# Optimization experiments

Measured on AMD Instinct MI355X. Metric: run time of the kernel, lower is better.

Reference implementation:

```python
import jax, jax.numpy as jnp
import numpy as np

N = 20000; E = 320000; IN = 128; H = 6; C = 64; HC = H * C; NC = 16; NG = 64


def _gatv2(x, src, dst, wl, bl, wr, br, att, bias, heads, out_c, concat):
    # PyG GATv2Conv (eval mode, share_weights=False, negative_slope=0.2)
    n = x.shape[0]
    xl = (x @ wl + bl).reshape(n, heads, out_c)   # source-side transform
    xr = (x @ wr + br).reshape(n, heads, out_c)   # target-side transform
    # edge-wise attention logits: leaky_relu(x_l[j] + x_r[i]) . att
    e = jnp.einsum('ehc,hc->eh', jax.nn.leaky_relu(xl[src] + xr[dst], 0.2), att)
    # segment softmax over incoming edges of each target node
    emax = jax.ops.segment_max(e, dst, num_segments=n)
    a = jnp.exp(e - emax[dst])
    denom = jax.ops.segment_sum(a, dst, num_segments=n)
    alpha = a / (denom[dst] + 1e-16)
    out = jax.ops.segment_sum(xl[src] * alpha[:, :, None], dst, num_segments=n)
    out = out.reshape(n, heads * out_c) if concat else out.mean(axis=1)
    return out + bias


def setup_inputs() -> dict:
    key = jax.random.key(0)
    ks = jax.random.split(key, 32)
    s = 0.05
    inp = {}
    inp['x'] = jax.random.normal(ks[0], (N, IN), jnp.float32)
    inp['edge_index'] = jax.random.randint(ks[1], (2, E), 0, N, dtype=jnp.int32)
    inp['batch'] = jnp.sort(jax.random.randint(ks[2], (N,), 0, NG, dtype=jnp.int32))
    # input projection (input_dim != hidden_dim * n_heads)
    inp['inp_w'] = jax.random.normal(ks[3], (IN, HC), jnp.float32) * s
    inp['inp_b'] = jnp.zeros((HC,), jnp.float32)
    # layer 0: IN -> (H, C), concat
    inp['l0_wl'] = jax.random.normal(ks[4], (IN, HC), jnp.float32) * s
    inp['l0_bl'] = jnp.zeros((HC,), jnp.float32)
    inp['l0_wr'] = jax.random.normal(ks[5], (IN, HC), jnp.float32) * s
    inp['l0_br'] = jnp.zeros((HC,), jnp.float32)
    inp['l0_att'] = jax.random.normal(ks[6], (H, C), jnp.float32) * s
    inp['l0_bias'] = jnp.zeros((HC,), jnp.float32)
    # layer 1: HC -> (H, C), concat
    inp['l1_wl'] = jax.random.normal(ks[7], (HC, HC), jnp.float32) * s
    inp['l1_bl'] = jnp.zeros((HC,), jnp.float32)
    inp['l1_wr'] = jax.random.normal(ks[8], (HC, HC), jnp.float32) * s
    inp['l1_br'] = jnp.zeros((HC,), jnp.float32)
    inp['l1_att'] = jax.random.normal(ks[9], (H, C), jnp.float32) * s
    inp['l1_bias'] = jnp.zeros((HC,), jnp.float32)
    # layer 2: HC -> (1, C), no concat (mean over the single head)
    inp['l2_wl'] = jax.random.normal(ks[10], (HC, C), jnp.float32) * s
    inp['l2_bl'] = jnp.zeros((C,), jnp.float32)
    inp['l2_wr'] = jax.random.normal(ks[11], (HC, C), jnp.float32) * s
    inp['l2_br'] = jnp.zeros((C,), jnp.float32)
    inp['l2_att'] = jax.random.normal(ks[12], (1, C), jnp.float32) * s
    inp['l2_bias'] = jnp.zeros((C,), jnp.float32)
    # residual projection HC -> C at the last layer (bias-free Linear)
    inp['res_w'] = jax.random.normal(ks[13], (HC, C), jnp.float32) * s
    # dense head: Linear(C,C) + BatchNorm1d(eval) + ReLU + Linear(C,NC)
    inp['d1_w'] = jax.random.normal(ks[14], (C, C), jnp.float32) * s
    inp['d1_b'] = jnp.zeros((C,), jnp.float32)
    inp['bn_g'] = jnp.ones((C,), jnp.float32)
    inp['bn_b'] = jnp.zeros((C,), jnp.float32)
    inp['bn_m'] = jnp.zeros((C,), jnp.float32)
    inp['bn_v'] = jnp.ones((C,), jnp.float32)
    inp['d2_w'] = jax.random.normal(ks[15], (C, NC), jnp.float32) * s
    inp['d2_b'] = jnp.zeros((NC,), jnp.float32)
    return inp


def reference(x, edge_index, batch, inp_w, inp_b,
              l0_wl, l0_bl, l0_wr, l0_br, l0_att, l0_bias,
              l1_wl, l1_bl, l1_wr, l1_br, l1_att, l1_bias,
              l2_wl, l2_bl, l2_wr, l2_br, l2_att, l2_bias,
              res_w, d1_w, d1_b, bn_g, bn_b, bn_m, bn_v, d2_w, d2_b):
    n = x.shape[0]
    sl = jnp.arange(n, dtype=edge_index.dtype)           # self-loops (PyG default)
    src = jnp.concatenate([edge_index[0], sl])
    dst = jnp.concatenate([edge_index[1], sl])
    x_res = x @ inp_w + inp_b
    h = jax.nn.elu(_gatv2(x, src, dst, l0_wl, l0_bl, l0_wr, l0_br, l0_att, l0_bias, H, C, True)) + x_res
    x_res = h
    h = jax.nn.elu(_gatv2(h, src, dst, l1_wl, l1_bl, l1_wr, l1_br, l1_att, l1_bias, H, C, True)) + x_res
    x_res = h
    h = jax.nn.elu(_gatv2(h, src, dst, l2_wl, l2_bl, l2_wr, l2_br, l2_att, l2_bias, 1, C, False)) + x_res @ res_w
    pooled = jax.ops.segment_sum(h, batch, num_segments=NG)
    z = pooled @ d1_w + d1_b
    z = (z - bn_m) / jnp.sqrt(bn_v + 1e-5) * bn_g + bn_b  # BatchNorm1d eval
    z = jax.nn.relu(z) @ d2_w + d2_b
    return h, z
```

## Files before the change

kernel.cpp:

```cpp
#include <hip/hip_runtime.h>
#include <hip/hip_bf16.h>
#include <math.h>

#define NN 20000
#define EE 320000
#define IND 128
#define HH 6
#define CC 64
#define HCC 384
#define NCC 16
#define NGG 64

typedef __bf16 bf16x8 __attribute__((ext_vector_type(8)));
typedef float f32x4 __attribute__((ext_vector_type(4)));
typedef float f32x2 __attribute__((ext_vector_type(2)));
typedef unsigned short ushort_t;
typedef unsigned int uint_t;

#define LOG2E 1.44269504088896f

__device__ inline ushort_t f2bf(float f) {
    union { float f; uint_t u; } x; x.f = f;
    uint_t r = (x.u + 0x7FFF + ((x.u >> 16) & 1)) >> 16;
    return (ushort_t)r;
}
__device__ inline void bf8cvt2(uint4 v, f32x2* f) {
    union { uint_t u; float x; } a, b;
    a.u = v.x << 16; b.u = v.x & 0xFFFF0000u; f[0] = (f32x2){a.x, b.x};
    a.u = v.y << 16; b.u = v.y & 0xFFFF0000u; f[1] = (f32x2){a.x, b.x};
    a.u = v.z << 16; b.u = v.z & 0xFFFF0000u; f[2] = (f32x2){a.x, b.x};
    a.u = v.w << 16; b.u = v.w & 0xFFFF0000u; f[3] = (f32x2){a.x, b.x};
}

template <int CTRL>
__device__ inline float dppadd(float x) {
    int y = __builtin_amdgcn_mov_dpp(__builtin_bit_cast(int, x), CTRL, 0xF, 0xF, true);
    return x + __builtin_bit_cast(float, y);
}

__device__ inline void load_lds16(const ushort_t* g, ushort_t* l) {
    __builtin_amdgcn_global_load_lds(
        (const __attribute__((address_space(1))) void*)g,
        (__attribute__((address_space(3))) void*)l, 16, 0, 0);
}

__device__ inline int xcd_swz(int lin, int nwg) {
    int q = nwg >> 3, r = nwg & 7;
    int xc = lin & 7, j = lin >> 3;
    return (xc < r ? xc * (q + 1) : r * (q + 1) + (xc - r) * q) + j;
}


__global__ void zero_init_kernel(int* counts, int* s6_tail, int* s1_tail,
                                 float* pooled, int n, int np) {
    int t = blockIdx.x * blockDim.x + threadIdx.x;
    if (t < n) counts[t] = 0;
    if (t < np) pooled[t] = 0.0f;
    if (t < 8) { s6_tail[t] = 0; s1_tail[t] = 0; }
}

__global__ void count_kernel(const int* __restrict__ ei, int* __restrict__ counts, int E) {
    int t = blockIdx.x * blockDim.x + threadIdx.x;
    if (t < E) atomicAdd(&counts[ei[E + t]], 1);
}

__global__ __launch_bounds__(1024) void scan_kernel(
    const int* __restrict__ counts, int* __restrict__ offsets,
    int* __restrict__ cursor, int n) {
    __shared__ int buf[NN];
    __shared__ int part[1024];
    int t = threadIdx.x;
    for (int idx = t; idx < n; idx += 1024) buf[idx] = counts[idx] + 1;
    __syncthreads();
    int per = (n + 1023) / 1024;
    int base = t * per;
    int sum = 0;
    for (int j = 0; j < per; ++j) {
        int idx = base + j;
        if (idx < n) sum += buf[idx];
    }
    part[t] = sum;
    __syncthreads();
    for (int off = 1; off < 1024; off <<= 1) {
        int v = (t >= off) ? part[t - off] : 0;
        __syncthreads();
        part[t] += v;
        __syncthreads();
    }
    int run = (t == 0) ? 0 : part[t - 1];
    for (int j = 0; j < per; ++j) {
        int idx = base + j;
        if (idx < n) {
            int deg = buf[idx];
            buf[idx] = run;
            run += deg;
        }
    }
    __syncthreads();
    for (int idx = t; idx < n; idx += 1024) {
        int v = buf[idx];
        offsets[idx] = v;
        cursor[idx] = v;
    }
    if (t == 1023) offsets[n] = run;
}

__global__ void fill_kernel(const int* __restrict__ ei, int* __restrict__ cursor,
                            int* __restrict__ srcs6, int* __restrict__ srcs1,
                            int E, int n) {
    int t = blockIdx.x * blockDim.x + threadIdx.x;
    if (t < E) {
        int s = ei[t];
        int d = ei[E + t];
        int slot = atomicAdd(&cursor[d], 1);
        srcs6[slot] = s * 1536;
        srcs1[slot] = s << 8;
    } else if (t < E + n) {
        int i = t - E;
        int slot = atomicAdd(&cursor[i], 1);
        srcs6[slot] = i * 1536;
        srcs1[slot] = i << 8;
    }
}

#define WBIG (1152 * IND)
#define WC1 (768 * HCC)
#define WC2 (192 * HCC)
#define XB_N (NN * IND)
#define PREP_TOTAL (WBIG + WC1 + WC2 + XB_N + 1152 + 768 + 192)

__global__ void prep_kernel(const float* __restrict__ x, const float* __restrict__ inp_w,
    const float* __restrict__ l0wl, const float* __restrict__ l0wr,
    const float* __restrict__ l1wl, const float* __restrict__ l1wr,
    const float* __restrict__ l2wl, const float* __restrict__ l2wr,
    const float* __restrict__ resw,
    const float* __restrict__ inp_b,
    const float* __restrict__ l0bl, const float* __restrict__ l0br,
    const float* __restrict__ l1bl, const float* __restrict__ l1br,
    const float* __restrict__ l2bl, const float* __restrict__ l2br,
    ushort_t* wBig, ushort_t* wC1, ushort_t* wC2, ushort_t* xb,
    float* bBig, float* bC1, float* bC2)
{
    int i = blockIdx.x * blockDim.x + threadIdx.x;
    if (i >= PREP_TOTAL) return;
    if (i < WBIG) {
        int col = i >> 7, k = i & 127;
        float v;
        if (col < 384)      v = inp_w[k * 384 + col];
        else if (col < 768) v = l0wl[k * 384 + (col - 384)];
        else                v = l0wr[k * 384 + (col - 768)];
        wBig[i] = f2bf(v); return;
    }
    i -= WBIG;
    if (i < WC1) {
        int col = i / 384, k = i - col * 384;
        float v = col < 384 ? l1wl[k * 384 + col] : l1wr[k * 384 + (col - 384)];
        wC1[i] = f2bf(v); return;
    }
    i -= WC1;
    if (i < WC2) {
        int col = i / 384, k = i - col * 384;
        float v;
        if (col < 64)       v = resw[k * 64 + col];
        else if (col < 128) v = l2wl[k * 64 + (col - 64)];
        else                v = l2wr[k * 64 + (col - 128)];
        wC2[i] = f2bf(v); return;
    }
    i -= WC2;
    if (i < XB_N) { xb[i] = f2bf(x[i]); return; }
    i -= XB_N;
    if (i < 1152) {
        float v;
        if (i < 384)      v = inp_b[i];
        else if (i < 768) v = l0bl[i - 384];
        else              v = l0br[i - 768];
        bBig[i] = v; return;
    }
    i -= 1152;
    if (i < 768) { bC1[i] = i < 384 ? l1bl[i] : l1br[i - 384]; return; }
    i -= 768;
    if (i < 192) {
        float v;
        if (i < 64)       v = 0.0f;
        else if (i < 128) v = l2bl[i - 64];
        else              v = l2br[i - 128];
        bC2[i] = v; return;
    }
}

__global__ __launch_bounds__(512) void gemm_mfma2(
    const ushort_t* __restrict__ A, const ushort_t* __restrict__ BT,
    const float* __restrict__ bias,
    ushort_t* __restrict__ Cb1, int ld1,
    ushort_t* __restrict__ Cb2, int ld2, int split,
    int M, int N, int K, int NT)
{
    __shared__ ushort_t Bs[2][2][128 * 32];
    int t = threadIdx.x;
    int w = t >> 6, L = t & 63;
    int nwg = gridDim.x * gridDim.y;
    int logical = xcd_swz(blockIdx.y * gridDim.x + blockIdx.x, nwg);
    int bx = logical % gridDim.x;
    int by = logical / gridDim.x;
    int m0 = bx * 256;
    int q = L >> 4, r16 = L & 15;
    int lr = L >> 2;
    int lc = ((L & 3) ^ ((lr >> 1) & 3)) * 8;
    int sw = (q ^ ((r16 >> 1) & 3)) * 8;
    int oB = (w * 16) * 32;

    int rA0 = min(m0 + w * 32 + r16, M - 1);
    int rA1 = min(m0 + w * 32 + 16 + r16, M - 1);
    const ushort_t* pA0base = A + (size_t)rA0 * K + q * 8;
    const ushort_t* pA1base = A + (size_t)rA1 * K + q * 8;

    for (int nt = 0; nt < NT; ++nt) {
        int n0 = (by * NT + nt) * 128;
        int rB = min(n0 + w * 16 + lr, N - 1);
        const ushort_t* gB = BT + (size_t)rB * K + lc;
        const ushort_t* pA0 = pA0base;
        const ushort_t* pA1 = pA1base;

        f32x4 acc[2][8];
#pragma unroll
        for (int a = 0; a < 2; ++a)
#pragma unroll
            for (int b = 0; b < 8; ++b) acc[a][b] = (f32x4){0.f, 0.f, 0.f, 0.f};

        load_lds16(gB, &Bs[0][0][oB]);
        load_lds16(gB + 32, &Bs[0][1][oB]);
        gB += 64;
        bf16x8 a0 = *(const bf16x8*)pA0;
        bf16x8 a2 = *(const bf16x8*)(pA0 + 32);
        bf16x8 a1 = *(const bf16x8*)pA1;
        bf16x8 a3 = *(const bf16x8*)(pA1 + 32);
        pA0 += 64; pA1 += 64;

        int buf = 0;
        for (int k0 = 0; k0 < K; k0 += 64) {
            __syncthreads();
            bool more = (k0 + 64 < K);
            if (more) {
                int nb = buf ^ 1;
                load_lds16(gB, &Bs[nb][0][oB]);
                load_lds16(gB + 32, &Bs[nb][1][oB]);
                gB += 64;
            }
            bf16x8 na0, na1, na2, na3;
            if (more) {
                na0 = *(const bf16x8*)pA0;
                na2 = *(const bf16x8*)(pA0 + 32);
                na1 = *(const bf16x8*)pA1;
                na3 = *(const bf16x8*)(pA1 + 32);
                pA0 += 64; pA1 += 64;
            }
#pragma unroll
            for (int ct = 0; ct < 8; ++ct) {
                bf16x8 blo = *(const bf16x8*)&Bs[buf][0][(ct * 16 + r16) * 32 + sw];
                bf16x8 bhi = *(const bf16x8*)&Bs[buf][1][(ct * 16 + r16) * 32 + sw];
                acc[0][ct] = __builtin_amdgcn_mfma_f32_16x16x32_bf16(blo, a0, acc[0][ct], 0, 0, 0);
                acc[1][ct] = __builtin_amdgcn_mfma_f32_16x16x32_bf16(blo, a1, acc[1][ct], 0, 0, 0);
                acc[0][ct] = __builtin_amdgcn_mfma_f32_16x16x32_bf16(bhi, a2, acc[0][ct], 0, 0, 0);
                acc[1][ct] = __builtin_amdgcn_mfma_f32_16x16x32_bf16(bhi, a3, acc[1][ct], 0, 0, 0);
            }
            if (more) { a0 = na0; a1 = na1; a2 = na2; a3 = na3; }
            buf ^= 1;
        }
#pragma unroll
        for (int rt = 0; rt < 2; ++rt) {
            int row = m0 + w * 32 + rt * 16 + r16;
            if (row >= M) continue;
#pragma unroll
            for (int ct = 0; ct < 8; ++ct) {
                int colb = n0 + ct * 16 + q * 4;
                if (colb >= N) continue;
                float4 bv = *(const float4*)(bias + colb);
                uint2 pk;
                pk.x = (uint_t)f2bf(acc[rt][ct][0] + bv.x) | ((uint_t)f2bf(acc[rt][ct][1] + bv.y) << 16);
                pk.y = (uint_t)f2bf(acc[rt][ct][2] + bv.z) | ((uint_t)f2bf(acc[rt][ct][3] + bv.w) << 16);
                if (colb < split)
                    *(uint2*)(Cb1 + (size_t)row * ld1 + colb) = pk;
                else
                    *(uint2*)(Cb2 + (size_t)row * ld2 + (colb - split)) = pk;
            }
        }
    }
}

__global__ __launch_bounds__(256) void gemm_mfma(
    const ushort_t* __restrict__ A, const ushort_t* __restrict__ BT,
    const float* __restrict__ bias,
    float* __restrict__ Cf, ushort_t* __restrict__ Cb1, int ld1,
    ushort_t* __restrict__ Cb2, int ld2, int split,
    int M, int N, int K)
{
    __shared__ ushort_t Bs[2][2][128 * 32];
    int t = threadIdx.x;
    int w = t >> 6, L = t & 63;
    int nwg = gridDim.x * gridDim.y;
    int logical = xcd_swz(blockIdx.y * gridDim.x + blockIdx.x, nwg);
    int m0 = (logical % gridDim.x) * 128;
    int n0 = (logical / gridDim.x) * 128;
    int q = L >> 4, r16 = L & 15;

    f32x4 acc[2][8];
#pragma unroll
    for (int a = 0; a < 2; ++a)
#pragma unroll
        for (int b = 0; b < 8; ++b) acc[a][b] = (f32x4){0.f, 0.f, 0.f, 0.f};

    int lr = L >> 2;
    int lc = ((L & 3) ^ ((lr >> 1) & 3)) * 8;
    int rB0 = min(n0 + w * 32 + lr, N - 1);
    int rB1 = min(n0 + w * 32 + 16 + lr, N - 1);
    const ushort_t* gB0 = BT + (size_t)rB0 * K + lc;
    const ushort_t* gB1 = BT + (size_t)rB1 * K + lc;
    int oB0 = (w * 32) * 32;
    int oB1 = (w * 32 + 16) * 32;

    int rA0 = min(m0 + w * 32 + r16, M - 1);
    int rA1 = min(m0 + w * 32 + 16 + r16, M - 1);
    const ushort_t* pA0 = A + (size_t)rA0 * K + q * 8;
    const ushort_t* pA1 = A + (size_t)rA1 * K + q * 8;

    int sw = (q ^ ((r16 >> 1) & 3)) * 8;

    load_lds16(gB0, &Bs[0][0][oB0]);
    load_lds16(gB1, &Bs[0][0][oB1]);
    load_lds16(gB0 + 32, &Bs[0][1][oB0]);
    load_lds16(gB1 + 32, &Bs[0][1][oB1]);
    gB0 += 64; gB1 += 64;
    bf16x8 a0 = *(const bf16x8*)pA0;
    bf16x8 a2 = *(const bf16x8*)(pA0 + 32);
    bf16x8 a1 = *(const bf16x8*)pA1;
    bf16x8 a3 = *(const bf16x8*)(pA1 + 32);
    pA0 += 64; pA1 += 64;

    int buf = 0;
    for (int k0 = 0; k0 < K; k0 += 64) {
        __syncthreads();
        bool more = (k0 + 64 < K);
        if (more) {
            int nb = buf ^ 1;
            load_lds16(gB0, &Bs[nb][0][oB0]);
            load_lds16(gB1, &Bs[nb][0][oB1]);
            load_lds16(gB0 + 32, &Bs[nb][1][oB0]);
            load_lds16(gB1 + 32, &Bs[nb][1][oB1]);
            gB0 += 64; gB1 += 64;
        }
        bf16x8 na0, na1, na2, na3;
        if (more) {
            na0 = *(const bf16x8*)pA0;
            na2 = *(const bf16x8*)(pA0 + 32);
            na1 = *(const bf16x8*)pA1;
            na3 = *(const bf16x8*)(pA1 + 32);
            pA0 += 64; pA1 += 64;
        }
#pragma unroll
        for (int ct = 0; ct < 8; ++ct) {
            bf16x8 blo = *(const bf16x8*)&Bs[buf][0][(ct * 16 + r16) * 32 + sw];
            bf16x8 bhi = *(const bf16x8*)&Bs[buf][1][(ct * 16 + r16) * 32 + sw];
            acc[0][ct] = __builtin_amdgcn_mfma_f32_16x16x32_bf16(blo, a0, acc[0][ct], 0, 0, 0);
            acc[1][ct] = __builtin_amdgcn_mfma_f32_16x16x32_bf16(blo, a1, acc[1][ct], 0, 0, 0);
            acc[0][ct] = __builtin_amdgcn_mfma_f32_16x16x32_bf16(bhi, a2, acc[0][ct], 0, 0, 0);
            acc[1][ct] = __builtin_amdgcn_mfma_f32_16x16x32_bf16(bhi, a3, acc[1][ct], 0, 0, 0);
        }
        if (more) { a0 = na0; a1 = na1; a2 = na2; a3 = na3; }
        buf ^= 1;
    }
#pragma unroll
    for (int rt = 0; rt < 2; ++rt) {
        int row = m0 + w * 32 + rt * 16 + r16;
        if (row >= M) continue;
#pragma unroll
        for (int ct = 0; ct < 8; ++ct) {
            int colb = n0 + ct * 16 + q * 4;
            if (colb >= N) continue;
            float4 bv = *(const float4*)(bias + colb);
            float v0 = acc[rt][ct][0] + bv.x;
            float v1 = acc[rt][ct][1] + bv.y;
            float v2 = acc[rt][ct][2] + bv.z;
            float v3 = acc[rt][ct][3] + bv.w;
            if (colb < split) {
                if (Cf) {
                    *(float4*)(Cf + (size_t)row * ld1 + colb) = make_float4(v0, v1, v2, v3);
                } else {
                    uint2 pk;
                    pk.x = (uint_t)f2bf(v0) | ((uint_t)f2bf(v1) << 16);
                    pk.y = (uint_t)f2bf(v2) | ((uint_t)f2bf(v3) << 16);
                    *(uint2*)(Cb1 + (size_t)row * ld1 + colb) = pk;
                }
            } else {
                uint2 pk;
                pk.x = (uint_t)f2bf(v0) | ((uint_t)f2bf(v1) << 16);
                pk.y = (uint_t)f2bf(v2) | ((uint_t)f2bf(v3) << 16);
                *(uint2*)(Cb2 + (size_t)row * ld2 + (colb - split)) = pk;
            }
        }
    }
}

__global__ __launch_bounds__(128) void gat6_kernel(
    const ushort_t* __restrict__ cat, const float* __restrict__ att,
    const float* __restrict__ bias, const ushort_t* __restrict__ resB,
    ushort_t* __restrict__ outB,
    const int* __restrict__ offsets, const int* __restrict__ srcs6, int n)
{
    int wid = (blockIdx.x * blockDim.x + threadIdx.x) >> 6;
    if (wid >= n) return;
    int lane = threadIdx.x & 63;
    int h = lane >> 3, c8 = lane & 7;
    bool hv = h < HH;
    int off = h * 64 + c8 * 8;
    int offL2 = (hv ? off : off - 384) * 2;
    int i = wid;
    int beg = __builtin_amdgcn_readfirstlane(offsets[i]);
    int end = __builtin_amdgcn_readfirstlane(offsets[i + 1]);
    int deg = end - beg;
    int P = (deg + 1) >> 1;
    const char* catc = (const char*)cat;

    f32x2 xr2[4], att2[4];
    {
        uint4 v = *(const uint4*)(catc + (size_t)i * 1536 + 768 + offL2);
        bf8cvt2(v, xr2);
    }
#pragma unroll
    for (int j = 0; j < 4; ++j) {
        int o = (offL2 >> 1) + 2 * j;
        att2[j] = (f32x2){att[o] * LOG2E, att[o + 1] * LOG2E};
    }

    float s = 0.0f;
    f32x2 acc2[4];
#pragma unroll
    for (int j = 0; j < 4; ++j) acc2[j] = (f32x2){0.f, 0.f};

    int bA0 = srcs6[beg], bB0 = srcs6[beg + 1];
    uint4 cA = *(const uint4*)(catc + (size_t)(uint_t)bA0 + offL2);
    uint4 cB = *(const uint4*)(catc + (size_t)(uint_t)bB0 + offL2);
    int iA1 = srcs6[beg + 2], iB1 = srcs6[beg + 3];

    for (int p = 0; p < P; ++p) {
        uint4 nA = cA, nB = cB;
        bool pre = (p + 1 < P);
        if (pre) {
            nA = *(const uint4*)(catc + (size_t)(uint_t)iA1 + offL2);
            nB = *(const uint4*)(catc + (size_t)(uint_t)iB1 + offL2);
            iA1 = srcs6[beg + 2 * p + 4];
            iB1 = srcs6[beg + 2 * p + 5];
        }
        f32x2 xlA[4], xlB[4];
        bf8cvt2(cA, xlA);
        bf8cvt2(cB, xlB);
        f32x2 pA2 = (f32x2){0.f, 0.f}, pB2 = (f32x2){0.f, 0.f};
#pragma unroll
        for (int j = 0; j < 4; ++j) {
            f32x2 ta = xlA[j] + xr2[j];
            ta = __builtin_elementwise_max(ta, ta * 0.2f);
            pA2 += ta * att2[j];
            f32x2 tb = xlB[j] + xr2[j];
            tb = __builtin_elementwise_max(tb, tb * 0.2f);
            pB2 += tb * att2[j];
        }
        float pA = pA2.x + pA2.y, pB = pB2.x + pB2.y;
        pA = dppadd<0xB1>(pA);
        pB = dppadd<0xB1>(pB);
        pA = dppadd<0x4E>(pA);
        pB = dppadd<0x4E>(pB);
        pA = dppadd<0x141>(pA);
        pB = dppadd<0x141>(pB);
        float wA = __builtin_amdgcn_exp2f(pA);
        float wB = (2 * p + 1 < deg) ? __builtin_amdgcn_exp2f(pB) : 0.0f;
        s += wA + wB;
        f32x2 wA2 = (f32x2){wA, wA}, wB2 = (f32x2){wB, wB};
#pragma unroll
        for (int j = 0; j < 4; ++j) {
            acc2[j] += wA2 * xlA[j];
            acc2[j] += wB2 * xlB[j];
        }
        cA = nA; cB = nB;
    }

    if (hv) {
        float inv = 1.0f / (s + 1e-16f);
        size_t ob = (size_t)i * HCC + off;
        uint4 rv = *(const uint4*)(resB + ob);
        f32x2 rr[4];
        bf8cvt2(rv, rr);
        ushort_t u[8];
#pragma unroll
        for (int j = 0; j < 4; ++j) {
            float v0 = acc2[j].x * inv + bias[off + 2 * j];
            float v1 = acc2[j].y * inv + bias[off + 2 * j + 1];
            v0 = v0 > 0.0f ? v0 : expm1f(v0);
            v1 = v1 > 0.0f ? v1 : expm1f(v1);
            u[2 * j]     = f2bf(v0 + rr[j].x);
            u[2 * j + 1] = f2bf(v1 + rr[j].y);
        }
        *(uint4*)(outB + ob) = *(uint4*)u;
    }
}

__global__ __launch_bounds__(128) void gat1_kernel(
    const ushort_t* __restrict__ cat, const float* __restrict__ att,
    const float* __restrict__ bias, const float* __restrict__ res,
    float* __restrict__ out,
    const int* __restrict__ offsets, const int* __restrict__ srcs1, int n)
{
    int wid = (blockIdx.x * blockDim.x + threadIdx.x) >> 6;
    if (wid >= n) return;
    int lane = threadIdx.x & 63;
    int e8 = lane >> 3, c8 = lane & 7;
    int i = wid;
    int beg = __builtin_amdgcn_readfirstlane(offsets[i]);
    int end = __builtin_amdgcn_readfirstlane(offsets[i + 1]);
    const char* catc = (const char*)cat;

    f32x2 xr2[4], att2[4];
    {
        uint4 v = *(const uint4*)(cat + (size_t)i * 128 + 64 + c8 * 8);
        bf8cvt2(v, xr2);
    }
#pragma unroll
    for (int j = 0; j < 4; ++j)
        att2[j] = (f32x2){att[c8 * 8 + 2 * j] * LOG2E, att[c8 * 8 + 2 * j + 1] * LOG2E};

    float s = 0.0f;
    f32x2 acc2[4];
#pragma unroll
    for (int j = 0; j < 4; ++j) acc2[j] = (f32x2){0.f, 0.f};

    const uint4 z = make_uint4(0u, 0u, 0u, 0u);
    int p = beg + e8;
    bool val = p < end;
    int b = val ? srcs1[p] : (i << 8);
    uint4 v = *(const uint4*)(catc + (size_t)(uint_t)b + c8 * 16);

    for (int p0 = beg; p0 < end; p0 += 8) {
        uint4 nv = z;
        bool nval = false;
        if (p0 + 8 < end) {
            int np = p0 + 8 + e8;
            nval = np < end;
            int nb = nval ? srcs1[np] : (i << 8);
            nv = *(const uint4*)(catc + (size_t)(uint_t)nb + c8 * 16);
        }
        f32x2 xl[4];
        bf8cvt2(v, xl);
        f32x2 pp2 = (f32x2){0.f, 0.f};
#pragma unroll
        for (int j = 0; j < 4; ++j) {
            f32x2 tv = xl[j] + xr2[j];
            tv = __builtin_elementwise_max(tv, tv * 0.2f);
            pp2 += tv * att2[j];
        }
        float partial = pp2.x + pp2.y;
        partial = dppadd<0xB1>(partial);
        partial = dppadd<0x4E>(partial);
        partial = dppadd<0x141>(partial);
        float wE = val ? __builtin_amdgcn_exp2f(partial) : 0.0f;
        s += wE;
        f32x2 w2 = (f32x2){wE, wE};
#pragma unroll
        for (int j = 0; j < 4; ++j) acc2[j] += w2 * xl[j];
        v = nv;
        val = nval;
    }

    s = dppadd<0x140>(s);
    s += __shfl_xor(s, 16, 64);
    s += __shfl_xor(s, 32, 64);
#pragma unroll
    for (int j = 0; j < 4; ++j) {
        acc2[j].x += __shfl_xor(acc2[j].x, 8, 64);
        acc2[j].y += __shfl_xor(acc2[j].y, 8, 64);
        acc2[j].x += __shfl_xor(acc2[j].x, 16, 64);
        acc2[j].y += __shfl_xor(acc2[j].y, 16, 64);
        acc2[j].x += __shfl_xor(acc2[j].x, 32, 64);
        acc2[j].y += __shfl_xor(acc2[j].y, 32, 64);
    }
    if (e8 == 0) {
        float inv = 1.0f / (s + 1e-16f);
        size_t ob = (size_t)i * CC + c8 * 8;
        float4 r0 = *(const float4*)(res + ob);
        float4 r1 = *(const float4*)(res + ob + 4);
        float rr[8] = {r0.x, r0.y, r0.z, r0.w, r1.x, r1.y, r1.z, r1.w};
        float av[8] = {acc2[0].x, acc2[0].y, acc2[1].x, acc2[1].y,
                       acc2[2].x, acc2[2].y, acc2[3].x, acc2[3].y};
#pragma unroll
        for (int j = 0; j < 8; ++j) {
            float v2 = av[j] * inv + bias[c8 * 8 + j];
            v2 = v2 > 0.0f ? v2 : expm1f(v2);
            av[j] = v2 + rr[j];
        }
        *(float4*)(out + ob) = make_float4(av[0], av[1], av[2], av[3]);
        *(float4*)(out + ob + 4) = make_float4(av[4], av[5], av[6], av[7]);
    }
}

__global__ __launch_bounds__(256) void pool_kernel(const float* __restrict__ h,
                                                   const int* __restrict__ batch,
                                                   float* __restrict__ pooled, int n) {
    int b = blockIdx.x;
    int g = b >> 2, qd = b & 3;
    int t = threadIdx.x;
    int w = t >> 6, lane = t & 63;
    int lo = 0, hi = n;
    while (lo < hi) { int mid = (lo + hi) >> 1; if (batch[mid] < g) lo = mid + 1; else hi = mid; }
    int start = lo;
    int hi2 = n;
    while (lo < hi2) { int mid = (lo + hi2) >> 1; if (batch[mid] < g + 1) lo = mid + 1; else hi2 = mid; }
    int endd = lo;
    int len = endd - start;
    int q0 = start + (len * qd) / 4;
    int q1 = start + (len * (qd + 1)) / 4;
    float acc = 0.0f;
    for (int r = q0 + w; r < q1; r += 4)
        acc += h[(size_t)r * 64 + lane];
    __shared__ float red[4][64];
    red[w][lane] = acc;
    __syncthreads();
    if (w == 0) {
        float v2 = red[0][lane] + red[1][lane] + red[2][lane] + red[3][lane];
        atomicAdd(&pooled[g * 64 + lane], v2);
    }
}

__global__ __launch_bounds__(256) void head_kernel(const float* __restrict__ pooled,
                            const float* __restrict__ d1w, const float* __restrict__ d1b,
                            const float* __restrict__ bng, const float* __restrict__ bnb,
                            const float* __restrict__ bnm, const float* __restrict__ bnv,
                            const float* __restrict__ d2w, const float* __restrict__ d2b,
                            float* __restrict__ zout) {
    __shared__ float pl[64 * 64];
    __shared__ float w1[64 * 64];
    __shared__ float w2[64 * NCC];
    __shared__ float z1[64 * 64];
    int t = threadIdx.x;
    for (int i = t * 4; i < 64 * 64; i += 1024) {
        *(float4*)&pl[i] = *(const float4*)&pooled[i];
        *(float4*)&w1[i] = *(const float4*)&d1w[i];
    }
    for (int i = t * 4; i < 64 * NCC; i += 1024)
        *(float4*)&w2[i] = *(const float4*)&d2w[i];
    __syncthreads();
    for (int idx = t; idx < 64 * 64; idx += 256) {
        int r = idx >> 6, c = idx & 63;
        float acc = d1b[c];
        for (int k = 0; k < 64; ++k) acc += pl[r * 64 + k] * w1[k * 64 + c];
        acc = (acc - bnm[c]) / sqrtf(bnv[c] + 1e-5f) * bng[c] + bnb[c];
        z1[idx] = acc > 0.0f ? acc : 0.0f;
    }
    __syncthreads();
    for (int idx = t; idx < 64 * NCC; idx += 256) {
        int r = idx >> 4, c = idx & 15;
        float acc = d2b[c];
        for (int k = 0; k < 64; ++k) acc += z1[r * 64 + k] * w2[k * NCC + c];
        zout[idx] = acc;
    }
}


extern "C" void kernel_launch(void* const* d_in, const int* in_sizes, int n_in,
                              void* d_out, int out_size, void* d_ws, size_t ws_size,
                              hipStream_t stream) {
    const int N = NN, E = EE, C = CC, HC = HCC, NG = NGG;
    const int EN = E + N;

    const float* x     = (const float*)d_in[0];
    const int*   ei    = (const int*)d_in[1];
    const int*   batch = (const int*)d_in[2];
    const float* inp_w = (const float*)d_in[3];
    const float* inp_b = (const float*)d_in[4];
    const float* l0_wl = (const float*)d_in[5];
    const float* l0_bl = (const float*)d_in[6];
    const float* l0_wr = (const float*)d_in[7];
    const float* l0_br = (const float*)d_in[8];
    const float* l0_att = (const float*)d_in[9];
    const float* l0_bias = (const float*)d_in[10];
    const float* l1_wl = (const float*)d_in[11];
    const float* l1_bl = (const float*)d_in[12];
    const float* l1_wr = (const float*)d_in[13];
    const float* l1_br = (const float*)d_in[14];
    const float* l1_att = (const float*)d_in[15];
    const float* l1_bias = (const float*)d_in[16];
    const float* l2_wl = (const float*)d_in[17];
    const float* l2_bl = (const float*)d_in[18];
    const float* l2_wr = (const float*)d_in[19];
    const float* l2_br = (const float*)d_in[20];
    const float* l2_att = (const float*)d_in[21];
    const float* l2_bias = (const float*)d_in[22];
    const float* res_w = (const float*)d_in[23];
    const float* d1_w = (const float*)d_in[24];
    const float* d1_b = (const float*)d_in[25];
    const float* bn_g = (const float*)d_in[26];
    const float* bn_b = (const float*)d_in[27];
    const float* bn_m = (const float*)d_in[28];
    const float* bn_v = (const float*)d_in[29];
    const float* d2_w = (const float*)d_in[30];
    const float* d2_b = (const float*)d_in[31];

    float* out = (float*)d_out;

    char* ws = (char*)d_ws;
    size_t off = 0;
    auto alloc = [&](size_t bytes) -> void* {
        void* p = ws + off;
        off += (bytes + 255) & ~(size_t)255;
        return p;
    };
    ushort_t* bufH_b  = (ushort_t*)alloc((size_t)N * HC * 2);
    ushort_t* cat01_b = (ushort_t*)alloc((size_t)N * 768 * 2 + 2048);
    ushort_t* xres_b  = (ushort_t*)alloc((size_t)N * HC * 2);
    ushort_t* cat2_b  = (ushort_t*)alloc((size_t)N * 128 * 2);
    float*    bufRes  = (float*)alloc((size_t)N * C * 4);
    ushort_t* xb      = (ushort_t*)alloc((size_t)N * IND * 2);
    ushort_t* wBig    = (ushort_t*)alloc((size_t)WBIG * 2);
    ushort_t* wC1     = (ushort_t*)alloc((size_t)WC1 * 2);
    ushort_t* wC2     = (ushort_t*)alloc((size_t)WC2 * 2);
    float*    bBig    = (float*)alloc((size_t)1152 * 4);
    float*    bC1     = (float*)alloc((size_t)768 * 4);
    float*    bC2     = (float*)alloc((size_t)192 * 4);
    int*      counts  = (int*)alloc((size_t)N * 4);
    int*      cursor  = (int*)alloc((size_t)N * 4);
    int*      offsets = (int*)alloc((size_t)(N + 1) * 4);
    int*      srcs6   = (int*)alloc((size_t)(EN + 8) * 4);
    int*      srcs1   = (int*)alloc((size_t)(EN + 8) * 4);
    float*    pooled  = (float*)alloc((size_t)NG * C * 4);

    zero_init_kernel<<<(N + 255) / 256, 256, 0, stream>>>(counts, srcs6 + EN, srcs1 + EN,
                                                          pooled, N, NG * C);
    count_kernel<<<(E + 255) / 256, 256, 0, stream>>>(ei, counts, E);
    scan_kernel<<<1, 1024, 0, stream>>>(counts, offsets, cursor, N);
    fill_kernel<<<(EN + 255) / 256, 256, 0, stream>>>(ei, cursor, srcs6, srcs1, E, N);
    prep_kernel<<<(PREP_TOTAL + 255) / 256, 256, 0, stream>>>(
        x, inp_w, l0_wl, l0_wr, l1_wl, l1_wr, l2_wl, l2_wr, res_w,
        inp_b, l0_bl, l0_br, l1_bl, l1_br, l2_bl, l2_br,
        wBig, wC1, wC2, xb, bBig, bC1, bC2);

    int mtiles256 = (N + 255) / 256;
    int mtiles = (N + 127) / 128;
    dim3 gblk(128);
    int gatBlocks = (N * 64 + 127) / 128;

    gemm_mfma2<<<dim3(mtiles256, 3), dim3(512), 0, stream>>>(xb, wBig, bBig,
        xres_b, HC, cat01_b, 768, 384, N, 1152, IND, 3);
    gat6_kernel<<<gatBlocks, gblk, 0, stream>>>(cat01_b, l0_att, l0_bias,
                                                xres_b, bufH_b, offsets, srcs6, N);
    gemm_mfma2<<<dim3(mtiles256, 3), dim3(512), 0, stream>>>(bufH_b, wC1, bC1,
        nullptr, 0, cat01_b, 768, 0, N, 768, HC, 2);
    gat6_kernel<<<gatBlocks, gblk, 0, stream>>>(cat01_b, l1_att, l1_bias,
                                                bufH_b, bufH_b, offsets, srcs6, N);
    gemm_mfma<<<dim3(mtiles, 2), dim3(256), 0, stream>>>(bufH_b, wC2, bC2,
        bufRes, nullptr, C, cat2_b, 128, 64, N, 192, HC);
    gat1_kernel<<<gatBlocks, gblk, 0, stream>>>(cat2_b, l2_att, l2_bias,
                                                bufRes, out, offsets, srcs1, N);
    pool_kernel<<<NG * 4, 256, 0, stream>>>(out, batch, pooled, N);
    head_kernel<<<1, 256, 0, stream>>>(pooled, d1_w, d1_b, bn_g, bn_b, bn_m, bn_v,
                                       d2_w, d2_b, out + (size_t)N * C);
}
```

Measured before the change: 402.6 us.

## Parallelize CSR offset scan across blocks, merge source index arrays, reorder GEMM tiles

```diff
diff --git a/kernel.cpp b/kernel.cpp
--- a/kernel.cpp
+++ b/kernel.cpp
@@ -51,12 +51,12 @@
 }
 
 
-__global__ void zero_init_kernel(int* counts, int* s6_tail, int* s1_tail,
+__global__ void zero_init_kernel(int* counts, int* srcs_tail,
                                  float* pooled, int n, int np) {
     int t = blockIdx.x * blockDim.x + threadIdx.x;
     if (t < n) counts[t] = 0;
     if (t < np) pooled[t] = 0.0f;
-    if (t < 8) { s6_tail[t] = 0; s1_tail[t] = 0; }
+    if (t < 8) srcs_tail[t] = 0;
 }
 
 __global__ void count_kernel(const int* __restrict__ ei, int* __restrict__ counts, int E) {
@@ -64,62 +64,58 @@
     if (t < E) atomicAdd(&counts[ei[E + t]], 1);
 }
 
-__global__ __launch_bounds__(1024) void scan_kernel(
+__global__ __launch_bounds__(256) void scan_local_kernel(
     const int* __restrict__ counts, int* __restrict__ offsets,
-    int* __restrict__ cursor, int n) {
-    __shared__ int buf[NN];
-    __shared__ int part[1024];
-    int t = threadIdx.x;
-    for (int idx = t; idx < n; idx += 1024) buf[idx] = counts[idx] + 1;
+    int* __restrict__ blockSums, int n) {
+    __shared__ int lp[256];
+    int t = threadIdx.x, b = blockIdx.x;
+    int i = b * 256 + t;
+    int v = (i < n) ? counts[i] + 1 : 0;
+    lp[t] = v;
     __syncthreads();
-    int per = (n + 1023) / 1024;
-    int base = t * per;
-    int sum = 0;
-    for (int j = 0; j < per; ++j) {
-        int idx = base + j;
-        if (idx < n) sum += buf[idx];
-    }
-    part[t] = sum;
+    for (int o = 1; o < 256; o <<= 1) {
+        int u = (t >= o) ? lp[t - o] : 0;
+        __syncthreads();
+        lp[t] += u;
+        __syncthreads();
+    }
+    if (t == 255) blockSums[b] = lp[255];
+    if (i < n) offsets[i] = lp[t] - v;
+}
+
+__global__ __launch_bounds__(256) void scan_fixup_kernel(
+    const int* __restrict__ blockSums,
+    int* __restrict__ offsets, int* __restrict__ cursor, int n, int nb) {
+    __shared__ int red[256];
+    int t = threadIdx.x, b = blockIdx.x;
+    red[t] = (t < b) ? blockSums[t] : 0;
     __syncthreads();
-    for (int off = 1; off < 1024; off <<= 1) {
-        int v = (t >= off) ? part[t - off] : 0;
+    for (int o = 128; o > 0; o >>= 1) {
+        if (t < o) red[t] += red[t + o];
         __syncthreads();
-        part[t] += v;
-        __syncthreads();
-    }
-    int run = (t == 0) ? 0 : part[t - 1];
-    for (int j = 0; j < per; ++j) {
-        int idx = base + j;
-        if (idx < n) {
-            int deg = buf[idx];
-            buf[idx] = run;
-            run += deg;
-        }
-    }
-    __syncthreads();
-    for (int idx = t; idx < n; idx += 1024) {
-        int v = buf[idx];
-        offsets[idx] = v;
-        cursor[idx] = v;
-    }
-    if (t == 1023) offsets[n] = run;
+    }
+    int prefix = red[0];
+    int i = b * 256 + t;
+    if (i < n) {
+        int val = offsets[i] + prefix;
+        offsets[i] = val;
+        cursor[i] = val;
+    }
+    if (b == nb - 1 && t == 0) offsets[n] = prefix + blockSums[b];
 }
 
 __global__ void fill_kernel(const int* __restrict__ ei, int* __restrict__ cursor,
-                            int* __restrict__ srcs6, int* __restrict__ srcs1,
-                            int E, int n) {
+                            int* __restrict__ srcs, int E, int n) {
     int t = blockIdx.x * blockDim.x + threadIdx.x;
     if (t < E) {
         int s = ei[t];
         int d = ei[E + t];
         int slot = atomicAdd(&cursor[d], 1);
-        srcs6[slot] = s * 1536;
-        srcs1[slot] = s << 8;
+        srcs[slot] = s << 8;
     } else if (t < E + n) {
         int i = t - E;
         int slot = atomicAdd(&cursor[i], 1);
-        srcs6[slot] = i * 1536;
-        srcs1[slot] = i << 8;
+        srcs[slot] = i << 8;
     }
 }
 
@@ -200,8 +196,8 @@
     int w = t >> 6, L = t & 63;
     int nwg = gridDim.x * gridDim.y;
     int logical = xcd_swz(blockIdx.y * gridDim.x + blockIdx.x, nwg);
-    int bx = logical % gridDim.x;
-    int by = logical / gridDim.x;
+    int bx = logical / gridDim.y;
+    int by = logical % gridDim.y;
     int m0 = bx * 256;
     int q = L >> 4, r16 = L & 15;
     int lr = L >> 2;
@@ -299,8 +295,8 @@
     int w = t >> 6, L = t & 63;
     int nwg = gridDim.x * gridDim.y;
     int logical = xcd_swz(blockIdx.y * gridDim.x + blockIdx.x, nwg);
-    int m0 = (logical % gridDim.x) * 128;
-    int n0 = (logical / gridDim.x) * 128;
+    int m0 = (logical / gridDim.y) * 128;
+    int n0 = (logical % gridDim.y) * 128;
     int q = L >> 4, r16 = L & 15;
 
     f32x4 acc[2][8];
@@ -404,7 +400,7 @@
     const ushort_t* __restrict__ cat, const float* __restrict__ att,
     const float* __restrict__ bias, const ushort_t* __restrict__ resB,
     ushort_t* __restrict__ outB,
-    const int* __restrict__ offsets, const int* __restrict__ srcs6, int n)
+    const int* __restrict__ offsets, const int* __restrict__ srcs, int n)
 {
     int wid = (blockIdx.x * blockDim.x + threadIdx.x) >> 6;
     if (wid >= n) return;
@@ -436,10 +432,10 @@
 #pragma unroll
     for (int j = 0; j < 4; ++j) acc2[j] = (f32x2){0.f, 0.f};
 
-    int bA0 = srcs6[beg], bB0 = srcs6[beg + 1];
+    int bA0 = srcs[beg] * 6, bB0 = srcs[beg + 1] * 6;
     uint4 cA = *(const uint4*)(catc + (size_t)(uint_t)bA0 + offL2);
     uint4 cB = *(const uint4*)(catc + (size_t)(uint_t)bB0 + offL2);
-    int iA1 = srcs6[beg + 2], iB1 = srcs6[beg + 3];
+    int iA1 = srcs[beg + 2] * 6, iB1 = srcs[beg + 3] * 6;
 
     for (int p = 0; p < P; ++p) {
         uint4 nA = cA, nB = cB;
@@ -447,8 +443,8 @@
         if (pre) {
             nA = *(const uint4*)(catc + (size_t)(uint_t)iA1 + offL2);
             nB = *(const uint4*)(catc + (size_t)(uint_t)iB1 + offL2);
-            iA1 = srcs6[beg + 2 * p + 4];
-            iB1 = srcs6[beg + 2 * p + 5];
+            iA1 = srcs[beg + 2 * p + 4] * 6;
+            iB1 = srcs[beg + 2 * p + 5] * 6;
         }
         f32x2 xlA[4], xlB[4];
         bf8cvt2(cA, xlA);
@@ -506,7 +502,7 @@
     const ushort_t* __restrict__ cat, const float* __restrict__ att,
     const float* __restrict__ bias, const float* __restrict__ res,
     float* __restrict__ out,
-    const int* __restrict__ offsets, const int* __restrict__ srcs1, int n)
+    const int* __restrict__ offsets, const int* __restrict__ srcs, int n)
 {
     int wid = (blockIdx.x * blockDim.x + threadIdx.x) >> 6;
     if (wid >= n) return;
@@ -534,7 +530,7 @@
     const uint4 z = make_uint4(0u, 0u, 0u, 0u);
     int p = beg + e8;
     bool val = p < end;
-    int b = val ? srcs1[p] : (i << 8);
+    int b = val ? srcs[p] : (i << 8);
     uint4 v = *(const uint4*)(catc + (size_t)(uint_t)b + c8 * 16);
 
     for (int p0 = beg; p0 < end; p0 += 8) {
@@ -543,7 +539,7 @@
         if (p0 + 8 < end) {
             int np = p0 + 8 + e8;
             nval = np < end;
-            int nb = nval ? srcs1[np] : (i << 8);
+            int nb = nval ? srcs[np] : (i << 8);
             nv = *(const uint4*)(catc + (size_t)(uint_t)nb + c8 * 16);
         }
         f32x2 xl[4];
@@ -725,15 +721,18 @@
     int*      counts  = (int*)alloc((size_t)N * 4);
     int*      cursor  = (int*)alloc((size_t)N * 4);
     int*      offsets = (int*)alloc((size_t)(N + 1) * 4);
-    int*      srcs6   = (int*)alloc((size_t)(EN + 8) * 4);
-    int*      srcs1   = (int*)alloc((size_t)(EN + 8) * 4);
+    int*      srcs    = (int*)alloc((size_t)(EN + 8) * 4);
+    int*      blockSums = (int*)alloc((size_t)256 * 4);
     float*    pooled  = (float*)alloc((size_t)NG * C * 4);
 
-    zero_init_kernel<<<(N + 255) / 256, 256, 0, stream>>>(counts, srcs6 + EN, srcs1 + EN,
+    const int SCAN_NB = (N + 255) / 256;
+
+    zero_init_kernel<<<(N + 255) / 256, 256, 0, stream>>>(counts, srcs + EN,
                                                           pooled, N, NG * C);
     count_kernel<<<(E + 255) / 256, 256, 0, stream>>>(ei, counts, E);
-    scan_kernel<<<1, 1024, 0, stream>>>(counts, offsets, cursor, N);
-    fill_kernel<<<(EN + 255) / 256, 256, 0, stream>>>(ei, cursor, srcs6, srcs1, E, N);
+    scan_local_kernel<<<SCAN_NB, 256, 0, stream>>>(counts, offsets, blockSums, N);
+    scan_fixup_kernel<<<SCAN_NB, 256, 0, stream>>>(blockSums, offsets, cursor, N, SCAN_NB);
+    fill_kernel<<<(EN + 255) / 256, 256, 0, stream>>>(ei, cursor, srcs, E, N);
     prep_kernel<<<(PREP_TOTAL + 255) / 256, 256, 0, stream>>>(
         x, inp_w, l0_wl, l0_wr, l1_wl, l1_wr, l2_wl, l2_wr, res_w,
         inp_b, l0_bl, l0_br, l1_bl, l1_br, l2_bl, l2_br,
@@ -747,15 +746,15 @@
     gemm_mfma2<<<dim3(mtiles256, 3), dim3(512), 0, stream>>>(xb, wBig, bBig,
         xres_b, HC, cat01_b, 768, 384, N, 1152, IND, 3);
     gat6_kernel<<<gatBlocks, gblk, 0, stream>>>(cat01_b, l0_att, l0_bias,
-                                                xres_b, bufH_b, offsets, srcs6, N);
+                                                xres_b, bufH_b, offsets, srcs, N);
     gemm_mfma2<<<dim3(mtiles256, 3), dim3(512), 0, stream>>>(bufH_b, wC1, bC1,
         nullptr, 0, cat01_b, 768, 0, N, 768, HC, 2);
     gat6_kernel<<<gatBlocks, gblk, 0, stream>>>(cat01_b, l1_att, l1_bias,
-                                                bufH_b, bufH_b, offsets, srcs6, N);
+                                                bufH_b, bufH_b, offsets, srcs, N);
     gemm_mfma<<<dim3(mtiles, 2), dim3(256), 0, stream>>>(bufH_b, wC2, bC2,
         bufRes, nullptr, C, cat2_b, 128, 64, N, 192, HC);
     gat1_kernel<<<gatBlocks, gblk, 0, stream>>>(cat2_b, l2_att, l2_bias,
-                                                bufRes, out, offsets, srcs1, N);
+                                                bufRes, out, offsets, srcs, N);
     pool_kernel<<<NG * 4, 256, 0, stream>>>(out, batch, pooled, N);
     head_kernel<<<1, 256, 0, stream>>>(pooled, d1_w, d1_b, bn_g, bn_b, bn_m, bn_v,
                                        d2_w, d2_b, out + (size_t)N * C);
```

New measurement: 394.2 us. -2.1%, faster.
